# Optimization experiments

Measured on AMD Instinct MI355X. Metric: run time of the kernel, lower is better.

## Reference

```python
import jax, jax.numpy as jnp
import numpy as np

N_NODES = 100000
N_EDGES = 3200000
IN_F, HID_F, OUT_F = 512, 64, 16


def setup_inputs() -> dict:
    key = jax.random.key(0)
    k1, k2, k3, k4 = jax.random.split(key, 4)
    x = jax.random.normal(k1, (N_NODES, IN_F), dtype=jnp.float32)
    edge_index = jax.random.randint(k2, (2, N_EDGES), 0, N_NODES, dtype=jnp.int64)
    W1 = jax.random.normal(k3, (IN_F, HID_F), dtype=jnp.float32) * (1.0 / np.sqrt(IN_F))
    b1 = jnp.zeros((HID_F,), dtype=jnp.float32)
    W2 = jax.random.normal(k4, (HID_F, OUT_F), dtype=jnp.float32) * (1.0 / np.sqrt(HID_F))
    b2 = jnp.zeros((OUT_F,), dtype=jnp.float32)
    return {"x": x, "edge_index": edge_index, "W1": W1, "b1": b1, "W2": W2, "b2": b2}


def _gcn_norm(edge_index, n_nodes):
    # add self-loops (GCNConv default), edge_weight = 1
    loop = jnp.arange(n_nodes, dtype=edge_index.dtype)
    src = jnp.concatenate([edge_index[0], loop])
    dst = jnp.concatenate([edge_index[1], loop])
    ones = jnp.ones(src.shape[0], dtype=jnp.float32)
    deg = jax.ops.segment_sum(ones, dst, num_segments=n_nodes)
    dinv = jnp.where(deg > 0, jax.lax.rsqrt(deg), 0.0)
    norm = dinv[src] * dinv[dst]  # symmetric normalization D^-1/2 A D^-1/2
    return src, dst, norm


def _gcn_conv(h, src, dst, norm, W, b, n_nodes):
    h = h @ W                                 # project first (small GEMM)
    msg = h[src] * norm[:, None]              # gather + scale  [E+N, F_out]
    agg = jax.ops.segment_sum(msg, dst, num_segments=n_nodes)  # scatter-add
    return agg + b


def reference(x, edge_index, W1, b1, W2, b2):
    n = x.shape[0]
    src, dst, norm = _gcn_norm(edge_index, n)
    h = jax.nn.relu(_gcn_conv(x, src, dst, norm, W1, b1, n))
    # F.dropout with training=False is identity (eval-mode reference)
    h = _gcn_conv(h, src, dst, norm, W2, b2, n)
    return jax.nn.log_softmax(h, axis=1)
```

## Files before the change

kernel.cpp:

```cpp
#include <hip/hip_runtime.h>

#define NN    100000
#define NE    3200000
#define INF_  512
#define HIDF  64
#define OUTF  16
#define BR    128
#define NBUCK ((NN + BR - 1) / BR)
#define NGRP  8
#define SLICE 704
#define BSLOT (NGRP * SLICE)
#define NCUR  (NBUCK * NGRP)
#define CPAD  16
#define NSLOT 72
#define EBLK  8192
#define NFB   ((NE + EBLK - 1) / EBLK)
#define GM    64
#define NGB   ((NN + GM - 1) / GM)

typedef __bf16 bf16x8 __attribute__((ext_vector_type(8)));
typedef float  f32x4  __attribute__((ext_vector_type(4)));

__device__ inline unsigned short f2bfu(float f) {
    unsigned u = __builtin_bit_cast(unsigned, f);
    u += 0x7FFFu + ((u >> 16) & 1u);
    return (unsigned short)(u >> 16);
}
__device__ inline __bf16 bfbits(unsigned short h) {
    return __builtin_bit_cast(__bf16, h);
}
__device__ inline float bf2f(unsigned short h) {
    unsigned u = (unsigned)h << 16;
    return __builtin_bit_cast(float, u);
}

__device__ inline void gll16(const float* g, void* l) {
    __builtin_amdgcn_global_load_lds(
        (const __attribute__((address_space(1))) unsigned int*)g,
        (__attribute__((address_space(3))) unsigned int*)l,
        16, 0, 0);
}

__global__ __launch_bounds__(256) void k_prep(const float* __restrict__ W1,
                                              unsigned short* __restrict__ w1c,
                                              int* __restrict__ bcur) {
    int b = blockIdx.x, t = threadIdx.x;
    if (b < 128) {
        int i = b * 256 + t;
        int k = i >> 6, n = i & 63;
        w1c[((k >> 2) * 64 + n) * 4 + (k & 3)] = f2bfu(W1[i]);
    } else {
        int i = (b - 128) * 256 + t;
        if (i < NCUR) bcur[i * CPAD] = (i >> 3) * BSLOT + (i & 7) * SLICE;
    }
}

__global__ __launch_bounds__(256) void k_main(const float* __restrict__ x,
                                              const unsigned short* __restrict__ w1c,
                                              const int* __restrict__ src,
                                              const int* __restrict__ dst,
                                              int* __restrict__ bcur,
                                              unsigned int* __restrict__ pairs,
                                              unsigned short* __restrict__ h1s) {
    __shared__ __align__(16) char smem[49152];
    int t = threadIdx.x;

    if (blockIdx.x < NFB) {
        int* hist  = (int*)smem;
        int* rbase = ((int*)smem) + NBUCK;
        int e0 = blockIdx.x * EBLK;
        int e1 = (e0 + EBLK < NE) ? e0 + EBLK : NE;
        int grp = (int)(((long long)blockIdx.x * NGRP) / NFB);

        for (int b = t; b < NBUCK; b += 256) hist[b] = 0;
        __syncthreads();
        for (int e = e0 + t; e < e1; e += 256)
            atomicAdd(&hist[dst[e] >> 7], 1);
        __syncthreads();
        for (int b = t; b < NBUCK; b += 256) {
            int c = hist[b];
            rbase[b] = c ? atomicAdd(&bcur[(b * NGRP + grp) * CPAD], c) : 0;
            hist[b] = 0;
        }
        __syncthreads();
        for (int e = e0 + t; e < e1; e += 256) {
            int s = src[e], d = dst[e];
            int b = d >> 7;
            int slot = atomicAdd(&hist[b], 1);
            pairs[rbase[b] + slot] = ((unsigned)s << 7) | (unsigned)(d & 127);
        }
        return;
    }

    unsigned short* bs = (unsigned short*)smem;
    float*          xt = (float*)(smem + 16384);
    int lane = t & 63;
    int w    = __builtin_amdgcn_readfirstlane(t >> 6);
    int m    = lane & 15;
    int kg   = lane >> 4;
    int mb   = (blockIdx.x - NFB) * GM;

    int rl_half = lane >> 5;
    int segl    = lane & 31;
    int rA  = w * 16 + m;
    int swz = rA & 7;

    f32x4 acc0 = {0.f,0.f,0.f,0.f}, acc1 = acc0, acc2 = acc0, acc3 = acc0;

    const uint4* w1c4 = (const uint4*)w1c;
    uint4* bs4 = (uint4*)bs;

    for (int kc = 0; kc < 4; ++kc) {
        if (kc) __syncthreads();
#pragma unroll
        for (int i = 0; i < 4; ++i)
            bs4[t + i * 256] = w1c4[kc * 1024 + t + i * 256];
#pragma unroll
        for (int i = 0; i < 8; ++i) {
            int rloc = w * 16 + i * 2 + rl_half;
            int rg   = mb + rloc; if (rg >= NN) rg = NN - 1;
            int sseg = segl ^ (rloc & 7);
            const float* gp = x + (size_t)rg * INF_ + kc * 128 + sseg * 4;
            gll16(gp, (char*)xt + (w * 8192 + i * 1024));
        }
        __syncthreads();

#pragma unroll
        for (int ks = 0; ks < 4; ++ks) {
            int s0g = ks * 8 + kg;
            float4 xa  = *(const float4*)&xt[rA * 128 + ((s0g ^ swz) << 2)];
            float4 xbv = *(const float4*)&xt[rA * 128 + (((s0g + 4) ^ swz) << 2)];
            bf16x8 A;
            A[0] = bfbits(f2bfu(xa.x));  A[1] = bfbits(f2bfu(xa.y));
            A[2] = bfbits(f2bfu(xa.z));  A[3] = bfbits(f2bfu(xa.w));
            A[4] = bfbits(f2bfu(xbv.x)); A[5] = bfbits(f2bfu(xbv.y));
            A[6] = bfbits(f2bfu(xbv.z)); A[7] = bfbits(f2bfu(xbv.w));

            int qq0 = ks * 8 + kg;
            int qq1 = qq0 + 4;
#pragma unroll
            for (int n0t = 0; n0t < 4; ++n0t) {
                ushort4 b0 = *(const ushort4*)&bs[(qq0 * 64 + n0t * 16 + m) * 4];
                ushort4 b1 = *(const ushort4*)&bs[(qq1 * 64 + n0t * 16 + m) * 4];
                bf16x8 B;
                B[0] = bfbits(b0.x); B[1] = bfbits(b0.y);
                B[2] = bfbits(b0.z); B[3] = bfbits(b0.w);
                B[4] = bfbits(b1.x); B[5] = bfbits(b1.y);
                B[6] = bfbits(b1.z); B[7] = bfbits(b1.w);
                f32x4 c = (n0t == 0) ? acc0 : (n0t == 1) ? acc1 : (n0t == 2) ? acc2 : acc3;
                c = __builtin_amdgcn_mfma_f32_16x16x32_bf16(A, B, c, 0, 0, 0);
                if      (n0t == 0) acc0 = c;
                else if (n0t == 1) acc1 = c;
                else if (n0t == 2) acc2 = c;
                else               acc3 = c;
            }
        }
    }

#pragma unroll
    for (int r = 0; r < 4; ++r) {
        int node = mb + w * 16 + kg * 4 + r;
        if (node < NN) {
            size_t o = (size_t)node * HIDF + m;
            h1s[o +  0] = f2bfu(acc0[r]);
            h1s[o + 16] = f2bfu(acc1[r]);
            h1s[o + 32] = f2bfu(acc2[r]);
            h1s[o + 48] = f2bfu(acc3[r]);
        }
    }
}

__global__ __launch_bounds__(256) void k_fillB(const int* __restrict__ bcur,
                                               const unsigned int* __restrict__ pairs,
                                               int* __restrict__ re,
                                               float* __restrict__ dinv,
                                               int* __restrict__ csr,
                                               unsigned short* __restrict__ h1s) {
    __shared__ int   cur_s[BR];
    __shared__ float dinv_s[BR];
    int b  = blockIdx.x;
    int t  = threadIdx.x;
    int n0 = b * BR;
    int ncount = ((n0 + BR < NN) ? BR : NN - n0);

    if (t < BR) cur_s[t] = (n0 + t) * NSLOT;
    __syncthreads();

    for (int g = 0; g < NGRP; ++g) {
        int s0 = b * BSLOT + g * SLICE;
        int s1 = bcur[(b * NGRP + g) * CPAD];
        for (int j = s0 + t; j < s1; j += 256) {
            unsigned int p = pairs[j];
            int pos = atomicAdd(&cur_s[p & 127u], 1);
            csr[pos] = (int)(p >> 7);
        }
    }
    __syncthreads();

    if (t < ncount) {
        int endp = cur_s[t];
        int n = n0 + t;
        float dv = rsqrtf((float)(endp - n * NSLOT + 1));
        re[n]    = endp;
        dinv[n]  = dv;
        dinv_s[t] = dv;
    }
    __syncthreads();

    for (int i = t; i < ncount * HIDF; i += 256) {
        unsigned idx = (unsigned)(n0 * HIDF + i);
        h1s[idx] = f2bfu(bf2f(h1s[idx]) * dinv_s[i >> 6]);
    }
}

__global__ __launch_bounds__(256) void k_hid2(const int* __restrict__ re,
                                              const int* __restrict__ csr,
                                              const float* __restrict__ dinv,
                                              const unsigned short* __restrict__ h1s,
                                              const float* __restrict__ b1,
                                              const float* __restrict__ W2,
                                              unsigned short* __restrict__ h2s) {
    __shared__ float w2s[HIDF * OUTF];
    __shared__ float b1s[HIDF];
    __shared__ float hbuf[4][HIDF];
    int t = threadIdx.x;
    for (int i = t; i < HIDF * OUTF; i += 256) w2s[i] = W2[i];
    if (t < HIDF) b1s[t] = b1[t];
    __syncthreads();

    int l = t & 63;
    int w = t >> 6;
    int g = l >> 4;
    int q = l & 15;
    int n = __builtin_amdgcn_readfirstlane(blockIdx.x * 4 + w);
    int row = n * NSLOT;
    int end = re[n];
    float dn = dinv[n];

    float a0 = 0.f, a1 = 0.f, a2 = 0.f, a3 = 0.f;

    int j = row;
    for (; j + 16 <= end; j += 16) {
        int4 scA = *(const int4*)&csr[j];
        int4 scB = *(const int4*)&csr[j + 4];
        int4 scC = *(const int4*)&csr[j + 8];
        int4 scD = *(const int4*)&csr[j + 12];
        int sA = (g & 2) ? ((g & 1) ? scA.w : scA.z) : ((g & 1) ? scA.y : scA.x);
        int sB = (g & 2) ? ((g & 1) ? scB.w : scB.z) : ((g & 1) ? scB.y : scB.x);
        int sC = (g & 2) ? ((g & 1) ? scC.w : scC.z) : ((g & 1) ? scC.y : scC.x);
        int sD = (g & 2) ? ((g & 1) ? scD.w : scD.z) : ((g & 1) ? scD.y : scD.x);
        ushort4 hA = *(const ushort4*)&h1s[(unsigned)(sA * HIDF + q * 4)];
        ushort4 hB = *(const ushort4*)&h1s[(unsigned)(sB * HIDF + q * 4)];
        ushort4 hC = *(const ushort4*)&h1s[(unsigned)(sC * HIDF + q * 4)];
        ushort4 hD = *(const ushort4*)&h1s[(unsigned)(sD * HIDF + q * 4)];
        a0 += (bf2f(hA.x) + bf2f(hB.x)) + (bf2f(hC.x) + bf2f(hD.x));
        a1 += (bf2f(hA.y) + bf2f(hB.y)) + (bf2f(hC.y) + bf2f(hD.y));
        a2 += (bf2f(hA.z) + bf2f(hB.z)) + (bf2f(hC.z) + bf2f(hD.z));
        a3 += (bf2f(hA.w) + bf2f(hB.w)) + (bf2f(hC.w) + bf2f(hD.w));
    }
    for (; j + 8 <= end; j += 8) {
        int4 scA = *(const int4*)&csr[j];
        int4 scB = *(const int4*)&csr[j + 4];
        int sA = (g & 2) ? ((g & 1) ? scA.w : scA.z) : ((g & 1) ? scA.y : scA.x);
        int sB = (g & 2) ? ((g & 1) ? scB.w : scB.z) : ((g & 1) ? scB.y : scB.x);
        ushort4 hA = *(const ushort4*)&h1s[(unsigned)(sA * HIDF + q * 4)];
        ushort4 hB = *(const ushort4*)&h1s[(unsigned)(sB * HIDF + q * 4)];
        a0 += bf2f(hA.x) + bf2f(hB.x);
        a1 += bf2f(hA.y) + bf2f(hB.y);
        a2 += bf2f(hA.z) + bf2f(hB.z);
        a3 += bf2f(hA.w) + bf2f(hB.w);
    }
    if (j + 4 <= end) {
        int4 sc = *(const int4*)&csr[j];
        int s = (g & 2) ? ((g & 1) ? sc.w : sc.z) : ((g & 1) ? sc.y : sc.x);
        ushort4 h = *(const ushort4*)&h1s[(unsigned)(s * HIDF + q * 4)];
        a0 += bf2f(h.x); a1 += bf2f(h.y); a2 += bf2f(h.z); a3 += bf2f(h.w);
        j += 4;
    }
    if (j + g < end) {
        int s = csr[j + g];
        ushort4 h = *(const ushort4*)&h1s[(unsigned)(s * HIDF + q * 4)];
        a0 += bf2f(h.x); a1 += bf2f(h.y); a2 += bf2f(h.z); a3 += bf2f(h.w);
    }

    a0 += __shfl_xor(a0, 16); a1 += __shfl_xor(a1, 16);
    a2 += __shfl_xor(a2, 16); a3 += __shfl_xor(a3, 16);
    a0 += __shfl_xor(a0, 32); a1 += __shfl_xor(a1, 32);
    a2 += __shfl_xor(a2, 32); a3 += __shfl_xor(a3, 32);

    ushort4 hs = *(const ushort4*)&h1s[(unsigned)(n * HIDF + q * 4)];
    a0 = fmaxf(fmaf(dn, a0 + bf2f(hs.x), b1s[q * 4 + 0]), 0.f);
    a1 = fmaxf(fmaf(dn, a1 + bf2f(hs.y), b1s[q * 4 + 1]), 0.f);
    a2 = fmaxf(fmaf(dn, a2 + bf2f(hs.z), b1s[q * 4 + 2]), 0.f);
    a3 = fmaxf(fmaf(dn, a3 + bf2f(hs.w), b1s[q * 4 + 3]), 0.f);
    if (g == 0) *(float4*)&hbuf[w][q * 4] = make_float4(a0, a1, a2, a3);
    __syncthreads();

    int o  = l & 15;
    int kg = l >> 4;
    const float* hb = hbuf[w];
    float s = 0.f;
#pragma unroll
    for (int i = 0; i < 16; ++i) {
        int k = kg * 16 + i;
        s = fmaf(hb[k], w2s[k * OUTF + o], s);
    }
    s += __shfl_xor(s, 16);
    s += __shfl_xor(s, 32);
    if (l < 16) h2s[(unsigned)(n * OUTF + o)] = f2bfu(dn * s);
}

__global__ __launch_bounds__(256) void k_out2(const int* __restrict__ re,
                                              const int* __restrict__ csr,
                                              const float* __restrict__ dinv,
                                              const unsigned short* __restrict__ h2s,
                                              const float* __restrict__ b2,
                                              float* __restrict__ out) {
    int t = blockIdx.x * 256 + threadIdx.x;
    int n = t >> 4;
    int f = t & 15;
    if (n >= NN) return;
    int row = n * NSLOT, end = re[n];
    float dn = dinv[n];
    float acc = bf2f(h2s[(unsigned)(n * OUTF + f)]);

    int j = row;
    for (; j + 8 <= end; j += 8) {
        int s0 = csr[j],     s1 = csr[j + 1], s2 = csr[j + 2], s3 = csr[j + 3];
        int s4 = csr[j + 4], s5 = csr[j + 5], s6 = csr[j + 6], s7 = csr[j + 7];
        float v0 = bf2f(h2s[(unsigned)(s0 * OUTF + f)]);
        float v1 = bf2f(h2s[(unsigned)(s1 * OUTF + f)]);
        float v2 = bf2f(h2s[(unsigned)(s2 * OUTF + f)]);
        float v3 = bf2f(h2s[(unsigned)(s3 * OUTF + f)]);
        float v4 = bf2f(h2s[(unsigned)(s4 * OUTF + f)]);
        float v5 = bf2f(h2s[(unsigned)(s5 * OUTF + f)]);
        float v6 = bf2f(h2s[(unsigned)(s6 * OUTF + f)]);
        float v7 = bf2f(h2s[(unsigned)(s7 * OUTF + f)]);
        acc += ((v0 + v1) + (v2 + v3)) + ((v4 + v5) + (v6 + v7));
    }
    for (; j + 4 <= end; j += 4) {
        int s0 = csr[j], s1 = csr[j + 1], s2 = csr[j + 2], s3 = csr[j + 3];
        float v0 = bf2f(h2s[(unsigned)(s0 * OUTF + f)]);
        float v1 = bf2f(h2s[(unsigned)(s1 * OUTF + f)]);
        float v2 = bf2f(h2s[(unsigned)(s2 * OUTF + f)]);
        float v3 = bf2f(h2s[(unsigned)(s3 * OUTF + f)]);
        acc += (v0 + v1) + (v2 + v3);
    }
    for (; j < end; ++j)
        acc += bf2f(h2s[(unsigned)(csr[j] * OUTF + f)]);

    float v = fmaf(dn, acc, b2[f]);

    float m = v;
#pragma unroll
    for (int mask = 1; mask < 16; mask <<= 1)
        m = fmaxf(m, __shfl_xor(m, mask, 16));
    float ex = __expf(v - m);
    float s  = ex;
#pragma unroll
    for (int mask = 1; mask < 16; mask <<= 1)
        s += __shfl_xor(s, mask, 16);
    out[(size_t)n * OUTF + f] = v - (m + __logf(s));
}

extern "C" void kernel_launch(void* const* d_in, const int* in_sizes, int n_in,
                              void* d_out, int out_size, void* d_ws, size_t ws_size,
                              hipStream_t stream) {
    const float* x  = (const float*)d_in[0];
    const int*   ei = (const int*)d_in[1];
    const float* W1 = (const float*)d_in[2];
    const float* b1 = (const float*)d_in[3];
    const float* W2 = (const float*)d_in[4];
    const float* b2 = (const float*)d_in[5];
    float*       out = (float*)d_out;

    char*  ws = (char*)d_ws;
    size_t o  = 0;
    auto alloc = [&](size_t bytes) {
        void* p = ws + o;
        o = (o + bytes + 1023) & ~(size_t)1023;
        return p;
    };
    int*            bcur  = (int*)           alloc((size_t)NCUR * CPAD * 4);
    int*            re    = (int*)           alloc((size_t)NN * 4);
    int*            csr   = (int*)           alloc((size_t)NN * NSLOT * 4);
    unsigned int*   pairs = (unsigned int*)  alloc((size_t)NBUCK * BSLOT * 4);
    float*          dinv  = (float*)         alloc((size_t)NN * 4);
    unsigned short* w1c   = (unsigned short*)alloc((size_t)INF_ * HIDF * 2);
    unsigned short* h1s   = (unsigned short*)alloc((size_t)NN * HIDF * 2);
    unsigned short* h2s   = (unsigned short*)alloc((size_t)NN * OUTF * 2);
    if (o > ws_size) return;

    const int* esrc = ei;
    const int* edst = ei + NE;

    k_prep  <<<128 + (NCUR + 255) / 256, 256, 0, stream>>>(W1, w1c, bcur);
    k_main  <<<NFB + NGB, 256, 0, stream>>>(x, w1c, esrc, edst, bcur, pairs, h1s);
    k_fillB <<<NBUCK, 256, 0, stream>>>(bcur, pairs, re, dinv, csr, h1s);
    k_hid2  <<<NN / 4, 256, 0, stream>>>(re, csr, dinv, h1s, b1, W2, h2s);
    k_out2  <<<(NN * OUTF + 255) / 256, 256, 0, stream>>>(re, csr, dinv, h2s, b2, out);
}
```

Measured before the change: 248.5 us.

## Double-buffer x tiles and preload full W1 into LDS in GEMM phase

The GEMM part of k_main now loads the whole bf16 W1 (64 KB) into shared memory once via global_load_lds and double-buffers the x tile. The next k-chunk is prefetched while the current one is consumed by MFMA. This removes the per-chunk W1 reload through registers and hides x load latency behind compute. Shared memory grows to 128 KB per block, which sharply reduces occupancy and also applies to the edge-bucketing blocks that share this kernel.

```diff
diff --git a/kernel.cpp b/kernel.cpp
--- a/kernel.cpp
+++ b/kernel.cpp
@@ -34,7 +34,7 @@
     return __builtin_bit_cast(float, u);
 }
 
-__device__ inline void gll16(const float* g, void* l) {
+__device__ inline void gll16(const void* g, void* l) {
     __builtin_amdgcn_global_load_lds(
         (const __attribute__((address_space(1))) unsigned int*)g,
         (__attribute__((address_space(3))) unsigned int*)l,
@@ -62,7 +62,7 @@
                                               int* __restrict__ bcur,
                                               unsigned int* __restrict__ pairs,
                                               unsigned short* __restrict__ h1s) {
-    __shared__ __align__(16) char smem[49152];
+    __shared__ __align__(16) char smem[131072];
     int t = threadIdx.x;
 
     if (blockIdx.x < NFB) {
@@ -92,8 +92,9 @@
         return;
     }
 
-    unsigned short* bs = (unsigned short*)smem;
-    float*          xt = (float*)(smem + 16384);
+    unsigned short* bs  = (unsigned short*)smem;
+    float*          xtA = (float*)(smem + 65536);
+    float*          xtB = (float*)(smem + 98304);
     int lane = t & 63;
     int w    = __builtin_amdgcn_readfirstlane(t >> 6);
     int m    = lane & 15;
@@ -107,36 +108,48 @@
 
     f32x4 acc0 = {0.f,0.f,0.f,0.f}, acc1 = acc0, acc2 = acc0, acc3 = acc0;
 
-    const uint4* w1c4 = (const uint4*)w1c;
-    uint4* bs4 = (uint4*)bs;
+    const char* w1cb = (const char*)w1c;
+#pragma unroll
+    for (int i = 0; i < 16; ++i) {
+        const void* gp = w1cb + w * 16384 + i * 1024 + lane * 16;
+        gll16(gp, (char*)bs + w * 16384 + i * 1024);
+    }
+#pragma unroll
+    for (int i = 0; i < 8; ++i) {
+        int rloc = w * 16 + i * 2 + rl_half;
+        int rg   = mb + rloc; if (rg >= NN) rg = NN - 1;
+        int sseg = segl ^ (rloc & 7);
+        const float* gp = x + (size_t)rg * INF_ + 0 * 128 + sseg * 4;
+        gll16(gp, (char*)xtA + (w * 8192 + i * 1024));
+    }
+    __syncthreads();
 
     for (int kc = 0; kc < 4; ++kc) {
-        if (kc) __syncthreads();
-#pragma unroll
-        for (int i = 0; i < 4; ++i)
-            bs4[t + i * 256] = w1c4[kc * 1024 + t + i * 256];
-#pragma unroll
-        for (int i = 0; i < 8; ++i) {
-            int rloc = w * 16 + i * 2 + rl_half;
-            int rg   = mb + rloc; if (rg >= NN) rg = NN - 1;
-            int sseg = segl ^ (rloc & 7);
-            const float* gp = x + (size_t)rg * INF_ + kc * 128 + sseg * 4;
-            gll16(gp, (char*)xt + (w * 8192 + i * 1024));
-        }
-        __syncthreads();
+        float* cur = (kc & 1) ? xtB : xtA;
+        float* nxt = (kc & 1) ? xtA : xtB;
+        if (kc < 3) {
+#pragma unroll
+            for (int i = 0; i < 8; ++i) {
+                int rloc = w * 16 + i * 2 + rl_half;
+                int rg   = mb + rloc; if (rg >= NN) rg = NN - 1;
+                int sseg = segl ^ (rloc & 7);
+                const float* gp = x + (size_t)rg * INF_ + (kc + 1) * 128 + sseg * 4;
+                gll16(gp, (char*)nxt + (w * 8192 + i * 1024));
+            }
+        }
 
 #pragma unroll
         for (int ks = 0; ks < 4; ++ks) {
             int s0g = ks * 8 + kg;
-            float4 xa  = *(const float4*)&xt[rA * 128 + ((s0g ^ swz) << 2)];
-            float4 xbv = *(const float4*)&xt[rA * 128 + (((s0g + 4) ^ swz) << 2)];
+            float4 xa  = *(const float4*)&cur[rA * 128 + ((s0g ^ swz) << 2)];
+            float4 xbv = *(const float4*)&cur[rA * 128 + (((s0g + 4) ^ swz) << 2)];
             bf16x8 A;
             A[0] = bfbits(f2bfu(xa.x));  A[1] = bfbits(f2bfu(xa.y));
             A[2] = bfbits(f2bfu(xa.z));  A[3] = bfbits(f2bfu(xa.w));
             A[4] = bfbits(f2bfu(xbv.x)); A[5] = bfbits(f2bfu(xbv.y));
             A[6] = bfbits(f2bfu(xbv.z)); A[7] = bfbits(f2bfu(xbv.w));
 
-            int qq0 = ks * 8 + kg;
+            int qq0 = (kc * 4 + ks) * 8 + kg;
             int qq1 = qq0 + 4;
 #pragma unroll
             for (int n0t = 0; n0t < 4; ++n0t) {
@@ -155,6 +168,7 @@
                 else               acc3 = c;
             }
         }
+        __syncthreads();
     }
 
 #pragma unroll
```

Result: no change. 252.8 us (+1.7%).
